# Optimization experiments

Hardware: AMD Instinct MI355X
Metric: run time of the kernel (lower is better)

The kernel has to match this reference:

```python
import jax, jax.numpy as jnp
import numpy as np

T, B, N, C = 4, 16, 256, 512
H = 8
HID = 4 * C
TAU = 2.0
EPS = 1e-5
SCALE = 0.125

@jax.custom_vjp
def spike_fn(x):
    return (x >= 0.0).astype(x.dtype)

def _spike_fwd(x):
    return spike_fn(x), x

def _spike_bwd(x, g):
    alpha = 4.0  # spikingjelly sigmoid surrogate default
    s = jax.nn.sigmoid(alpha * x)
    return (g * alpha * s * (1.0 - s),)

spike_fn.defvjp(_spike_fwd, _spike_bwd)

def lif(x_seq, v_th=1.0):
    # Multi-step LIF: v += (x - v)/tau (decay_input, v_reset=0), hard reset, detach_reset
    def step(v, xt):
        v = v + (xt - v) / TAU
        s = spike_fn(v - v_th)
        v = v * (1.0 - jax.lax.stop_gradient(s))
        return v, s
    _, out = jax.lax.scan(step, jnp.zeros_like(x_seq[0]), x_seq)
    return out

def lin_bn(x2d, w, b, g, beta):
    # Linear then BatchNorm1d (training mode, per-channel stats over all rows).
    # BN on (TB, Cout, N) over (batch, N) == BN on flattened (TB*N, Cout) over axis 0.
    y = x2d @ w.T + b
    mu = jnp.mean(y, axis=0)
    var = jnp.var(y, axis=0)
    return g * (y - mu) * jax.lax.rsqrt(var + EPS) + beta

def setup_inputs() -> dict:
    key = jax.random.key(0)
    ks = jax.random.split(key, 10)
    d = {
        "x": jax.random.normal(ks[0], (T, B, N, C), jnp.float32),
        "s_x": jax.random.normal(ks[1], (T, B, N, C), jnp.float32),
    }
    def lin(k, cout, cin):
        return jax.random.normal(k, (cout, cin), jnp.float32) * 0.02
    d["qw"] = lin(ks[2], C, C); d["qb"] = jnp.zeros((C,), jnp.float32)
    d["qg"] = jnp.ones((C,), jnp.float32); d["qbeta"] = jnp.zeros((C,), jnp.float32)
    d["kw"] = lin(ks[3], C, C); d["kb"] = jnp.zeros((C,), jnp.float32)
    d["kg"] = jnp.ones((C,), jnp.float32); d["kbeta"] = jnp.zeros((C,), jnp.float32)
    d["vw"] = lin(ks[4], C, C); d["vb"] = jnp.zeros((C,), jnp.float32)
    d["vg"] = jnp.ones((C,), jnp.float32); d["vbeta"] = jnp.zeros((C,), jnp.float32)
    d["pw"] = lin(ks[5], C, C); d["pb"] = jnp.zeros((C,), jnp.float32)
    d["pg"] = jnp.ones((C,), jnp.float32); d["pbeta"] = jnp.zeros((C,), jnp.float32)
    d["f1w"] = lin(ks[6], HID, C); d["f1b"] = jnp.zeros((HID,), jnp.float32)
    d["f1g"] = jnp.ones((HID,), jnp.float32); d["f1beta"] = jnp.zeros((HID,), jnp.float32)
    d["f2w"] = lin(ks[7], C, HID); d["f2b"] = jnp.zeros((C,), jnp.float32)
    d["f2g"] = jnp.ones((C,), jnp.float32); d["f2beta"] = jnp.zeros((C,), jnp.float32)
    return d

def _block(x, s_x, qw, qb, qg, qbeta, kw, kb, kg, kbeta, vw, vb, vg, vbeta,
           pw, pb, pg, pbeta, f1w, f1b, f1g, f1beta, f2w, f2b, f2g, f2beta):
    Dh = C // H
    xf = x.reshape(T * B * N, C)
    # SSA (s_x is unused in the source forward)
    q = lif(lin_bn(xf, qw, qb, qg, qbeta).reshape(T, B, N, C))
    k = lif(lin_bn(xf, kw, kb, kg, kbeta).reshape(T, B, N, C))
    v = lin_bn(xf, vw, vb, vg, vbeta).reshape(T, B, N, C)  # v has no LIF in source
    q = q.reshape(T, B, N, H, Dh).transpose(0, 1, 3, 2, 4)  # tbhnd
    k = k.reshape(T, B, N, H, Dh).transpose(0, 1, 3, 2, 4)
    v = v.reshape(T, B, N, H, Dh).transpose(0, 1, 3, 2, 4)
    attn = jnp.einsum('tbhnd,tbhmd->tbhnm', q, k) * SCALE  # no softmax
    o = jnp.einsum('tbhnm,tbhmd->tbhnd', attn, v)
    o = o.transpose(0, 1, 3, 2, 4).reshape(T * B * N, C)
    o = lin_bn(o, pw, pb, pg, pbeta).reshape(T, B, N, C)
    x = x + o
    # MLP
    xf2 = x.reshape(T * B * N, C)
    h = lif(lin_bn(xf2, f1w, f1b, f1g, f1beta).reshape(T, B, N, HID))
    m = lif(lin_bn(h.reshape(T * B * N, HID), f2w, f2b, f2g, f2beta).reshape(T, B, N, C))
    return x + m

def reference(x, s_x, qw, qb, qg, qbeta, kw, kb, kg, kbeta, vw, vb, vg, vbeta,
              pw, pb, pg, pbeta, f1w, f1b, f1g, f1beta, f2w, f2b, f2g, f2beta):
    return _block(x, s_x, qw, qb, qg, qbeta, kw, kb, kg, kbeta, vw, vb, vg, vbeta,
                  pw, pb, pg, pbeta, f1w, f1b, f1g, f1beta, f2w, f2b, f2g, f2beta)
```

## Files before the change

kernel.cpp:

```cpp
#include <hip/hip_runtime.h>
#include <cstdint>

#define T_ 4
#define B_ 16
#define N_ 256
#define C_ 512
#define H_ 8
#define HID_ 2048
#define M_ (T_*B_*N_)
#define BNP_ (B_*N_)

__global__ __launch_bounds__(256, 2)
void gemm_f32_t128(const float* __restrict__ A, const float* __restrict__ W,
                   const float* __restrict__ bias, float* __restrict__ Y,
                   int Nc, int K) {
  __shared__ float As[2][16][132];
  __shared__ float Ws[2][16][132];
  const int tid  = threadIdx.x;
  const int row0 = blockIdx.y * 128;
  const int col0 = blockIdx.x * 128;
  const int tx = tid & 15, ty = tid >> 4;
  const int ar = tid >> 2;
  const int ac = (tid & 3) << 2;

  float acc[8][8];
  #pragma unroll
  for (int i = 0; i < 8; ++i)
    #pragma unroll
    for (int j = 0; j < 8; ++j) acc[i][j] = 0.f;

  const float* Ap0 = A + (size_t)(row0 + ar) * K + ac;
  const float* Ap1 = A + (size_t)(row0 + ar + 64) * K + ac;
  const float* Wp0 = W + (size_t)(col0 + ar) * K + ac;
  const float* Wp1 = W + (size_t)(col0 + ar + 64) * K + ac;

  float4 pa0 = *(const float4*)Ap0;
  float4 pa1 = *(const float4*)Ap1;
  float4 pw0 = *(const float4*)Wp0;
  float4 pw1 = *(const float4*)Wp1;
  As[0][ac+0][ar] = pa0.x; As[0][ac+1][ar] = pa0.y; As[0][ac+2][ar] = pa0.z; As[0][ac+3][ar] = pa0.w;
  As[0][ac+0][ar+64] = pa1.x; As[0][ac+1][ar+64] = pa1.y; As[0][ac+2][ar+64] = pa1.z; As[0][ac+3][ar+64] = pa1.w;
  Ws[0][ac+0][ar] = pw0.x; Ws[0][ac+1][ar] = pw0.y; Ws[0][ac+2][ar] = pw0.z; Ws[0][ac+3][ar] = pw0.w;
  Ws[0][ac+0][ar+64] = pw1.x; Ws[0][ac+1][ar+64] = pw1.y; Ws[0][ac+2][ar+64] = pw1.z; Ws[0][ac+3][ar+64] = pw1.w;
  __syncthreads();

  int buf = 0;
  for (int k0 = 0; k0 < K; k0 += 16) {
    const bool last = (k0 + 16 >= K);
    if (!last) {
      pa0 = *(const float4*)(Ap0 + k0 + 16);
      pa1 = *(const float4*)(Ap1 + k0 + 16);
      pw0 = *(const float4*)(Wp0 + k0 + 16);
      pw1 = *(const float4*)(Wp1 + k0 + 16);
    }
    #pragma unroll
    for (int kk = 0; kk < 16; ++kk) {
      float a[8], b[8];
      *(float4*)&a[0] = *(const float4*)&As[buf][kk][ty*4];
      *(float4*)&a[4] = *(const float4*)&As[buf][kk][64 + ty*4];
      *(float4*)&b[0] = *(const float4*)&Ws[buf][kk][tx*4];
      *(float4*)&b[4] = *(const float4*)&Ws[buf][kk][64 + tx*4];
      #pragma unroll
      for (int i = 0; i < 8; ++i)
        #pragma unroll
        for (int j = 0; j < 8; ++j)
          acc[i][j] = fmaf(a[i], b[j], acc[i][j]);
    }
    if (!last) {
      int nb = buf ^ 1;
      As[nb][ac+0][ar] = pa0.x; As[nb][ac+1][ar] = pa0.y; As[nb][ac+2][ar] = pa0.z; As[nb][ac+3][ar] = pa0.w;
      As[nb][ac+0][ar+64] = pa1.x; As[nb][ac+1][ar+64] = pa1.y; As[nb][ac+2][ar+64] = pa1.z; As[nb][ac+3][ar+64] = pa1.w;
      Ws[nb][ac+0][ar] = pw0.x; Ws[nb][ac+1][ar] = pw0.y; Ws[nb][ac+2][ar] = pw0.z; Ws[nb][ac+3][ar] = pw0.w;
      Ws[nb][ac+0][ar+64] = pw1.x; Ws[nb][ac+1][ar+64] = pw1.y; Ws[nb][ac+2][ar+64] = pw1.z; Ws[nb][ac+3][ar+64] = pw1.w;
      __syncthreads();
      buf = nb;
    }
  }

  #pragma unroll
  for (int ih = 0; ih < 2; ++ih)
    #pragma unroll
    for (int i = 0; i < 4; ++i) {
      size_t r = (size_t)(row0 + ih*64 + ty*4 + i);
      #pragma unroll
      for (int jh = 0; jh < 2; ++jh) {
        int c = col0 + jh*64 + tx*4;
        float4 o4;
        o4.x = acc[ih*4+i][jh*4+0] + bias[c+0];
        o4.y = acc[ih*4+i][jh*4+1] + bias[c+1];
        o4.z = acc[ih*4+i][jh*4+2] + bias[c+2];
        o4.w = acc[ih*4+i][jh*4+3] + bias[c+3];
        *(float4*)(Y + r * Nc + c) = o4;
      }
    }
}

__global__ __launch_bounds__(256, 2)
void gemm_f32_qk(const float* __restrict__ A,
                 const float* __restrict__ Wq, const float* __restrict__ bq,
                 const float* __restrict__ Wk, const float* __restrict__ bk,
                 float* __restrict__ Yq, float* __restrict__ Yk,
                 int Nc, int K) {
  __shared__ float As[2][16][68];
  __shared__ float Wqs[2][16][132];
  __shared__ float Wks[2][16][132];
  const int tid  = threadIdx.x;
  const int row0 = blockIdx.y * 64;
  const int col0 = blockIdx.x * 128;
  const int tx = tid & 15, ty = tid >> 4;
  const int ar = tid >> 2;
  const int ac = (tid & 3) << 2;

  float accq[4][8], acck[4][8];
  #pragma unroll
  for (int i = 0; i < 4; ++i)
    #pragma unroll
    for (int j = 0; j < 8; ++j) { accq[i][j] = 0.f; acck[i][j] = 0.f; }

  const float* Ap   = A  + (size_t)(row0 + ar) * K + ac;
  const float* Wqp0 = Wq + (size_t)(col0 + ar) * K + ac;
  const float* Wqp1 = Wq + (size_t)(col0 + ar + 64) * K + ac;
  const float* Wkp0 = Wk + (size_t)(col0 + ar) * K + ac;
  const float* Wkp1 = Wk + (size_t)(col0 + ar + 64) * K + ac;

  float4 pa  = *(const float4*)Ap;
  float4 pq0 = *(const float4*)Wqp0;
  float4 pq1 = *(const float4*)Wqp1;
  float4 pk0 = *(const float4*)Wkp0;
  float4 pk1 = *(const float4*)Wkp1;
  As[0][ac+0][ar] = pa.x; As[0][ac+1][ar] = pa.y; As[0][ac+2][ar] = pa.z; As[0][ac+3][ar] = pa.w;
  Wqs[0][ac+0][ar] = pq0.x; Wqs[0][ac+1][ar] = pq0.y; Wqs[0][ac+2][ar] = pq0.z; Wqs[0][ac+3][ar] = pq0.w;
  Wqs[0][ac+0][ar+64] = pq1.x; Wqs[0][ac+1][ar+64] = pq1.y; Wqs[0][ac+2][ar+64] = pq1.z; Wqs[0][ac+3][ar+64] = pq1.w;
  Wks[0][ac+0][ar] = pk0.x; Wks[0][ac+1][ar] = pk0.y; Wks[0][ac+2][ar] = pk0.z; Wks[0][ac+3][ar] = pk0.w;
  Wks[0][ac+0][ar+64] = pk1.x; Wks[0][ac+1][ar+64] = pk1.y; Wks[0][ac+2][ar+64] = pk1.z; Wks[0][ac+3][ar+64] = pk1.w;
  __syncthreads();

  int buf = 0;
  for (int k0 = 0; k0 < K; k0 += 16) {
    const bool last = (k0 + 16 >= K);
    if (!last) {
      pa  = *(const float4*)(Ap   + k0 + 16);
      pq0 = *(const float4*)(Wqp0 + k0 + 16);
      pq1 = *(const float4*)(Wqp1 + k0 + 16);
      pk0 = *(const float4*)(Wkp0 + k0 + 16);
      pk1 = *(const float4*)(Wkp1 + k0 + 16);
    }
    #pragma unroll
    for (int kk = 0; kk < 16; ++kk) {
      float4 av = *(const float4*)&As[buf][kk][ty*4];
      float a[4] = {av.x, av.y, av.z, av.w};
      float b[8];
      *(float4*)&b[0] = *(const float4*)&Wqs[buf][kk][tx*4];
      *(float4*)&b[4] = *(const float4*)&Wqs[buf][kk][64 + tx*4];
      #pragma unroll
      for (int i = 0; i < 4; ++i)
        #pragma unroll
        for (int j = 0; j < 8; ++j)
          accq[i][j] = fmaf(a[i], b[j], accq[i][j]);
      *(float4*)&b[0] = *(const float4*)&Wks[buf][kk][tx*4];
      *(float4*)&b[4] = *(const float4*)&Wks[buf][kk][64 + tx*4];
      #pragma unroll
      for (int i = 0; i < 4; ++i)
        #pragma unroll
        for (int j = 0; j < 8; ++j)
          acck[i][j] = fmaf(a[i], b[j], acck[i][j]);
    }
    if (!last) {
      int nb = buf ^ 1;
      As[nb][ac+0][ar] = pa.x; As[nb][ac+1][ar] = pa.y; As[nb][ac+2][ar] = pa.z; As[nb][ac+3][ar] = pa.w;
      Wqs[nb][ac+0][ar] = pq0.x; Wqs[nb][ac+1][ar] = pq0.y; Wqs[nb][ac+2][ar] = pq0.z; Wqs[nb][ac+3][ar] = pq0.w;
      Wqs[nb][ac+0][ar+64] = pq1.x; Wqs[nb][ac+1][ar+64] = pq1.y; Wqs[nb][ac+2][ar+64] = pq1.z; Wqs[nb][ac+3][ar+64] = pq1.w;
      Wks[nb][ac+0][ar] = pk0.x; Wks[nb][ac+1][ar] = pk0.y; Wks[nb][ac+2][ar] = pk0.z; Wks[nb][ac+3][ar] = pk0.w;
      Wks[nb][ac+0][ar+64] = pk1.x; Wks[nb][ac+1][ar+64] = pk1.y; Wks[nb][ac+2][ar+64] = pk1.z; Wks[nb][ac+3][ar+64] = pk1.w;
      __syncthreads();
      buf = nb;
    }
  }

  #pragma unroll
  for (int i = 0; i < 4; ++i) {
    size_t r = (size_t)(row0 + ty*4 + i);
    #pragma unroll
    for (int jh = 0; jh < 2; ++jh) {
      int c = col0 + jh*64 + tx*4;
      float4 oq, ok;
      oq.x = accq[i][jh*4+0] + bq[c+0];
      oq.y = accq[i][jh*4+1] + bq[c+1];
      oq.z = accq[i][jh*4+2] + bq[c+2];
      oq.w = accq[i][jh*4+3] + bq[c+3];
      *(float4*)(Yq + r * Nc + c) = oq;
      ok.x = acck[i][jh*4+0] + bk[c+0];
      ok.y = acck[i][jh*4+1] + bk[c+1];
      ok.z = acck[i][jh*4+2] + bk[c+2];
      ok.w = acck[i][jh*4+3] + bk[c+3];
      *(float4*)(Yk + r * Nc + c) = ok;
    }
  }
}

__global__ __launch_bounds__(256, 2)
void gemm_f64_v3(const float* __restrict__ A, const float* __restrict__ W,
                 const float* __restrict__ bias, float* __restrict__ Y,
                 int Nc, int K) {
  __shared__ double As[2][16][68];
  __shared__ double Ws[2][16][132];
  const int tid  = threadIdx.x;
  const int row0 = blockIdx.y * 64;
  const int col0 = blockIdx.x * 128;
  const int tx = tid & 15, ty = tid >> 4;
  const int lr = tid >> 2;
  const int lk = (tid & 3) << 2;

  double acc[4][8];
  #pragma unroll
  for (int i = 0; i < 4; ++i)
    #pragma unroll
    for (int j = 0; j < 8; ++j) acc[i][j] = 0.0;

  const float* Ap  = A + (size_t)(row0 + lr) * K + lk;
  const float* Wp0 = W + (size_t)(col0 + lr) * K + lk;
  const float* Wp1 = W + (size_t)(col0 + lr + 64) * K + lk;

  float4 pa  = *(const float4*)Ap;
  float4 pw0 = *(const float4*)Wp0;
  float4 pw1 = *(const float4*)Wp1;
  As[0][lk+0][lr] = (double)pa.x; As[0][lk+1][lr] = (double)pa.y;
  As[0][lk+2][lr] = (double)pa.z; As[0][lk+3][lr] = (double)pa.w;
  Ws[0][lk+0][lr] = (double)pw0.x; Ws[0][lk+1][lr] = (double)pw0.y;
  Ws[0][lk+2][lr] = (double)pw0.z; Ws[0][lk+3][lr] = (double)pw0.w;
  Ws[0][lk+0][lr+64] = (double)pw1.x; Ws[0][lk+1][lr+64] = (double)pw1.y;
  Ws[0][lk+2][lr+64] = (double)pw1.z; Ws[0][lk+3][lr+64] = (double)pw1.w;
  __syncthreads();

  int buf = 0;
  for (int k0 = 0; k0 < K; k0 += 16) {
    const bool last = (k0 + 16 >= K);
    if (!last) {
      pa  = *(const float4*)(Ap  + k0 + 16);
      pw0 = *(const float4*)(Wp0 + k0 + 16);
      pw1 = *(const float4*)(Wp1 + k0 + 16);
    }
    #pragma unroll
    for (int kk = 0; kk < 16; ++kk) {
      double a[4], b[8];
      *(double2*)&a[0] = *(const double2*)&As[buf][kk][ty*4];
      *(double2*)&a[2] = *(const double2*)&As[buf][kk][ty*4+2];
      *(double2*)&b[0] = *(const double2*)&Ws[buf][kk][tx*2];
      *(double2*)&b[2] = *(const double2*)&Ws[buf][kk][32 + tx*2];
      *(double2*)&b[4] = *(const double2*)&Ws[buf][kk][64 + tx*2];
      *(double2*)&b[6] = *(const double2*)&Ws[buf][kk][96 + tx*2];
      #pragma unroll
      for (int i = 0; i < 4; ++i)
        #pragma unroll
        for (int j = 0; j < 8; ++j)
          acc[i][j] = fma(a[i], b[j], acc[i][j]);
    }
    if (!last) {
      int nb = buf ^ 1;
      As[nb][lk+0][lr] = (double)pa.x; As[nb][lk+1][lr] = (double)pa.y;
      As[nb][lk+2][lr] = (double)pa.z; As[nb][lk+3][lr] = (double)pa.w;
      Ws[nb][lk+0][lr] = (double)pw0.x; Ws[nb][lk+1][lr] = (double)pw0.y;
      Ws[nb][lk+2][lr] = (double)pw0.z; Ws[nb][lk+3][lr] = (double)pw0.w;
      Ws[nb][lk+0][lr+64] = (double)pw1.x; Ws[nb][lk+1][lr+64] = (double)pw1.y;
      Ws[nb][lk+2][lr+64] = (double)pw1.z; Ws[nb][lk+3][lr+64] = (double)pw1.w;
      __syncthreads();
      buf = nb;
    }
  }

  #pragma unroll
  for (int i = 0; i < 4; ++i) {
    size_t r = (size_t)(row0 + ty*4 + i);
    #pragma unroll
    for (int g = 0; g < 4; ++g) {
      int c = col0 + g*32 + tx*2;
      float2 o2;
      o2.x = (float)(acc[i][g*2+0] + (double)bias[c+0]);
      o2.y = (float)(acc[i][g*2+1] + (double)bias[c+1]);
      *(float2*)(Y + r * Nc + c) = o2;
    }
  }
}

__global__ __launch_bounds__(256)
void col_stats_partial(const float* __restrict__ Y, int Nc,
                       float* __restrict__ psum, float* __restrict__ psq) {
  const int r0 = blockIdx.x * 32;
  for (int c = threadIdx.x; c < Nc; c += 256) {
    float s = 0.f, q = 0.f;
    const float* p = Y + (size_t)r0 * Nc + c;
    for (int r = 0; r < 32; ++r) {
      float v = p[(size_t)r * Nc];
      s += v;
      q = fmaf(v, v, q);
    }
    psum[(size_t)blockIdx.x * Nc + c] = s;
    psq [(size_t)blockIdx.x * Nc + c] = q;
  }
}

__global__ void col_stats_final(const float* __restrict__ psum, const float* __restrict__ psq,
                                int Nc, const float* __restrict__ g, const float* __restrict__ beta,
                                float* __restrict__ chp) {
  int c = blockIdx.x * blockDim.x + threadIdx.x;
  if (c >= Nc) return;
  double s = 0.0, q = 0.0;
  for (int p = 0; p < 512; ++p) {
    s += (double)psum[(size_t)p * Nc + c];
    q += (double)psq [(size_t)p * Nc + c];
  }
  double mean = s / (double)M_;
  double var  = q / (double)M_ - mean * mean;
  float alpha = g[c] / sqrtf((float)var + 1e-5f);
  chp[2*c]   = alpha;
  chp[2*c+1] = fmaf(-(float)mean, alpha, beta[c]);
}

__global__ void col_stats_final_f64(const float* __restrict__ psum, const float* __restrict__ psq,
                                    int Nc, const float* __restrict__ g, const float* __restrict__ beta,
                                    double* __restrict__ chpd) {
  int c = blockIdx.x * blockDim.x + threadIdx.x;
  if (c >= Nc) return;
  double s = 0.0, q = 0.0;
  for (int p = 0; p < 512; ++p) {
    s += (double)psum[(size_t)p * Nc + c];
    q += (double)psq [(size_t)p * Nc + c];
  }
  double mean = s / (double)M_;
  double var  = q / (double)M_ - mean * mean;
  double alpha = (double)g[c] / sqrt(var + 1e-5);
  chpd[2*c]   = alpha;
  chpd[2*c+1] = (double)beta[c] - mean * alpha;
}

__global__ __launch_bounds__(256)
void bnlif_mask(const float* __restrict__ Y, const float* __restrict__ chp,
                unsigned long long* __restrict__ mask) {
  int lane = threadIdx.x & 63;
  int u  = blockIdx.x * 4 + (threadIdx.x >> 6);
  int bn = u >> 3, cg = u & 7;
  int c  = cg * 64 + lane;
  float alpha = chp[2*c], bb = chp[2*c+1];
  float v = 0.f;
  #pragma unroll
  for (int t = 0; t < 4; ++t) {
    float y  = Y[((size_t)(t * BNP_ + bn)) * C_ + c];
    float uu = fmaf(y, alpha, bb);
    v = v + (uu - v) * 0.5f;
    bool sp = (v >= 1.0f);
    unsigned long long m = __ballot(sp);
    if (sp) v = 0.f;
    if (lane == 0) mask[((size_t)(t * BNP_ + bn)) * H_ + cg] = m;
  }
}

__global__ void bn_apply_f64(const float* __restrict__ Y, const double* __restrict__ chpd,
                             float* __restrict__ out) {
  const long total4 = (long)M_ * C_ / 4;
  for (long i = (long)blockIdx.x * blockDim.x + threadIdx.x; i < total4;
       i += (long)gridDim.x * blockDim.x) {
    int c4 = (int)(i & (C_/4 - 1)) * 4;
    float4 y = ((const float4*)Y)[i];
    float4 r;
    r.x = (float)fma((double)y.x, chpd[2*(c4+0)], chpd[2*(c4+0)+1]);
    r.y = (float)fma((double)y.y, chpd[2*(c4+1)], chpd[2*(c4+1)+1]);
    r.z = (float)fma((double)y.z, chpd[2*(c4+2)], chpd[2*(c4+2)+1]);
    r.w = (float)fma((double)y.w, chpd[2*(c4+3)], chpd[2*(c4+3)+1]);
    ((float4*)out)[i] = r;
  }
}

__global__ void bn_residual_f64(const float* __restrict__ Y, const double* __restrict__ chpd,
                                const float* __restrict__ x, float* __restrict__ out) {
  const long total4 = (long)M_ * C_ / 4;
  for (long i = (long)blockIdx.x * blockDim.x + threadIdx.x; i < total4;
       i += (long)gridDim.x * blockDim.x) {
    int c4 = (int)(i & (C_/4 - 1)) * 4;
    float4 y = ((const float4*)Y)[i];
    float4 xv = ((const float4*)x)[i];
    float4 r;
    r.x = (float)((double)xv.x + fma((double)y.x, chpd[2*(c4+0)], chpd[2*(c4+0)+1]));
    r.y = (float)((double)xv.y + fma((double)y.y, chpd[2*(c4+1)], chpd[2*(c4+1)+1]));
    r.z = (float)((double)xv.z + fma((double)y.z, chpd[2*(c4+2)], chpd[2*(c4+2)+1]));
    r.w = (float)((double)xv.w + fma((double)y.w, chpd[2*(c4+3)], chpd[2*(c4+3)+1]));
    ((float4*)out)[i] = r;
  }
}

__global__ __launch_bounds__(256)
void bnlif_inplace(float* __restrict__ Y, const float* __restrict__ chp) {
  int c  = blockIdx.x * 256 + threadIdx.x;
  int bn = blockIdx.y;
  float alpha = chp[2*c], bb = chp[2*c+1];
  float v = 0.f;
  #pragma unroll
  for (int t = 0; t < 4; ++t) {
    size_t idx = ((size_t)(t * BNP_ + bn)) * HID_ + c;
    float uu = fmaf(Y[idx], alpha, bb);
    v = v + (uu - v) * 0.5f;
    bool sp = (v >= 1.f);
    Y[idx] = sp ? 1.f : 0.f;
    if (sp) v = 0.f;
  }
}

__global__ __launch_bounds__(256)
void bnlif_final(const float* __restrict__ Y, const float* __restrict__ chp,
                 const float* __restrict__ xo, float* __restrict__ out) {
  int c  = blockIdx.x * 256 + threadIdx.x;
  int bn = blockIdx.y;
  float alpha = chp[2*c], bb = chp[2*c+1];
  float v = 0.f;
  #pragma unroll
  for (int t = 0; t < 4; ++t) {
    size_t idx = ((size_t)(t * BNP_ + bn)) * C_ + c;
    float uu = fmaf(Y[idx], alpha, bb);
    v = v + (uu - v) * 0.5f;
    bool sp = (v >= 1.f);
    out[idx] = xo[idx] + (sp ? 1.f : 0.f);
    if (sp) v = 0.f;
  }
}

__global__ __launch_bounds__(256)
void attn_kernel_f64(const unsigned long long* __restrict__ qmask,
                     const unsigned long long* __restrict__ kmask,
                     const float* __restrict__ v, float* __restrict__ o) {
  __shared__ unsigned long long km[256];
  __shared__ float vt[256][64];
  int rb  = blockIdx.x & 3;
  int tbh = blockIdx.x >> 2;
  int h   = tbh & 7, tb = tbh >> 3;
  int tid = threadIdx.x;

  km[tid] = kmask[(size_t)(tb * 256 + tid) * H_ + h];
  const float* vbase = v + (size_t)tb * 256 * C_ + h * 64;
  #pragma unroll
  for (int i = 0; i < 16; ++i) {
    int f = i * 256 + tid;
    int r = f >> 4, c4 = f & 15;
    *(float4*)&vt[r][c4 * 4] = *(const float4*)(vbase + (size_t)r * C_ + c4 * 4);
  }
  int lane = tid & 63, w = tid >> 6;
  int nr = lane & 15, dg = lane >> 4;
  int n  = rb * 64 + w * 16 + nr;
  unsigned long long qm = qmask[(size_t)(tb * 256 + n) * H_ + h];
  __syncthreads();

  double acc[16];
  #pragma unroll
  for (int j = 0; j < 16; ++j) acc[j] = 0.0;

  for (int m = 0; m < 256; ++m) {
    double s = (double)__popcll(qm & km[m]) * 0.125;
    #pragma unroll
    for (int j = 0; j < 4; ++j) {
      float4 vv = *(const float4*)&vt[m][dg * 16 + j * 4];
      acc[j*4+0] = fma(s, (double)vv.x, acc[j*4+0]);
      acc[j*4+1] = fma(s, (double)vv.y, acc[j*4+1]);
      acc[j*4+2] = fma(s, (double)vv.z, acc[j*4+2]);
      acc[j*4+3] = fma(s, (double)vv.w, acc[j*4+3]);
    }
  }
  float* orow = o + (size_t)(tb * 256 + n) * C_ + h * 64 + dg * 16;
  #pragma unroll
  for (int j = 0; j < 4; ++j)
    *(float4*)(orow + j * 4) = make_float4((float)acc[j*4], (float)acc[j*4+1],
                                           (float)acc[j*4+2], (float)acc[j*4+3]);
}

extern "C" void kernel_launch(void* const* d_in, const int* in_sizes, int n_in,
                              void* d_out, int out_size, void* d_ws, size_t ws_size,
                              hipStream_t stream) {
  const float* x    = (const float*)d_in[0];
  const float* qw   = (const float*)d_in[2];
  const float* qb   = (const float*)d_in[3];
  const float* qg   = (const float*)d_in[4];
  const float* qbe  = (const float*)d_in[5];
  const float* kw   = (const float*)d_in[6];
  const float* kb   = (const float*)d_in[7];
  const float* kg   = (const float*)d_in[8];
  const float* kbe  = (const float*)d_in[9];
  const float* vw   = (const float*)d_in[10];
  const float* vb   = (const float*)d_in[11];
  const float* vg   = (const float*)d_in[12];
  const float* vbe  = (const float*)d_in[13];
  const float* pw   = (const float*)d_in[14];
  const float* pb   = (const float*)d_in[15];
  const float* pg   = (const float*)d_in[16];
  const float* pbe  = (const float*)d_in[17];
  const float* f1w  = (const float*)d_in[18];
  const float* f1b  = (const float*)d_in[19];
  const float* f1g  = (const float*)d_in[20];
  const float* f1be = (const float*)d_in[21];
  const float* f2w  = (const float*)d_in[22];
  const float* f2b  = (const float*)d_in[23];
  const float* f2g  = (const float*)d_in[24];
  const float* f2be = (const float*)d_in[25];

  char* ws = (char*)d_ws;
  float* bufY = (float*)(ws);
  float* bufK = bufY + 8388608;
  float* bufV = (float*)(ws + 134217728ull);
  float* bufO = (float*)(ws + 167772160ull);
  unsigned long long* qmask = (unsigned long long*)(ws + 201326592ull);
  unsigned long long* kmask = (unsigned long long*)(ws + 202375168ull);
  float* psum = (float*)(ws + 203423744ull);
  float* psq  = (float*)(ws + 207618048ull);
  float* chp  = (float*)(ws + 211812352ull);
  double* chpd = (double*)(ws + 211828736ull);

  float* out = (float*)d_out;

  gemm_f32_qk<<<dim3(4,256), 256, 0, stream>>>(x, qw, qb, kw, kb, bufY, bufK, C_, C_);
  col_stats_partial<<<512, 256, 0, stream>>>(bufY, C_, psum, psq);
  col_stats_final<<<2, 256, 0, stream>>>(psum, psq, C_, qg, qbe, chp);
  bnlif_mask<<<8192, 256, 0, stream>>>(bufY, chp, qmask);
  col_stats_partial<<<512, 256, 0, stream>>>(bufK, C_, psum, psq);
  col_stats_final<<<2, 256, 0, stream>>>(psum, psq, C_, kg, kbe, chp);
  bnlif_mask<<<8192, 256, 0, stream>>>(bufK, chp, kmask);
  gemm_f64_v3<<<dim3(4,256), 256, 0, stream>>>(x, vw, vb, bufY, C_, C_);
  col_stats_partial<<<512, 256, 0, stream>>>(bufY, C_, psum, psq);
  col_stats_final_f64<<<2, 256, 0, stream>>>(psum, psq, C_, vg, vbe, chpd);
  bn_apply_f64<<<2048, 256, 0, stream>>>(bufY, chpd, bufV);
  attn_kernel_f64<<<2048, 256, 0, stream>>>(qmask, kmask, bufV, bufO);
  gemm_f64_v3<<<dim3(4,256), 256, 0, stream>>>(bufO, pw, pb, bufY, C_, C_);
  col_stats_partial<<<512, 256, 0, stream>>>(bufY, C_, psum, psq);
  col_stats_final_f64<<<2, 256, 0, stream>>>(psum, psq, C_, pg, pbe, chpd);
  bn_residual_f64<<<2048, 256, 0, stream>>>(bufY, chpd, x, bufO);
  gemm_f32_t128<<<dim3(16,128), 256, 0, stream>>>(bufO, f1w, f1b, bufY, HID_, C_);
  col_stats_partial<<<512, 256, 0, stream>>>(bufY, HID_, psum, psq);
  col_stats_final<<<8, 256, 0, stream>>>(psum, psq, HID_, f1g, f1be, chp);
  bnlif_inplace<<<dim3(8,4096), 256, 0, stream>>>(bufY, chp);
  gemm_f32_t128<<<dim3(4,128), 256, 0, stream>>>(bufY, f2w, f2b, bufV, C_, HID_);
  col_stats_partial<<<512, 256, 0, stream>>>(bufV, C_, psum, psq);
  col_stats_final<<<2, 256, 0, stream>>>(psum, psq, C_, f2g, f2be, chp);
  bnlif_final<<<dim3(2,4096), 256, 0, stream>>>(bufV, chp, bufO, out);
}
```

Measured before the change: 1.937 ms.

## Pack MLP hidden spikes into bitmasks and run sparse f2 GEMM; widen f1 tile

The hidden LIF now writes a 64-bit ballot bitmask per row and 64 channels instead of a dense 0/1 float matrix. The second MLP linear becomes a sparse gather-accumulate that adds only the weight rows whose spike bit is set, so it skips multiplies by zero and reads far less activation memory. The f1 GEMM tile is also widened to 128x256 with a 8x16 accumulator per thread to improve reuse. The tradeoffs are divergent, data-dependent loops in the sparse kernel, a different summation order from the dense GEMM, and higher register pressure in the wider f1 tile.

Result: slower. 2.433 ms (+25.6%).

```diff
diff --git a/kernel.cpp b/kernel.cpp
--- a/kernel.cpp
+++ b/kernel.cpp
@@ -11,37 +11,43 @@
 #define BNP_ (B_*N_)
 
 __global__ __launch_bounds__(256, 2)
-void gemm_f32_t128(const float* __restrict__ A, const float* __restrict__ W,
+void gemm_f32_t256(const float* __restrict__ A, const float* __restrict__ W,
                    const float* __restrict__ bias, float* __restrict__ Y,
                    int Nc, int K) {
   __shared__ float As[2][16][132];
-  __shared__ float Ws[2][16][132];
+  __shared__ float Ws[2][16][260];
   const int tid  = threadIdx.x;
   const int row0 = blockIdx.y * 128;
-  const int col0 = blockIdx.x * 128;
+  const int col0 = blockIdx.x * 256;
   const int tx = tid & 15, ty = tid >> 4;
   const int ar = tid >> 2;
   const int ac = (tid & 3) << 2;
 
-  float acc[8][8];
+  float acc[8][16];
   #pragma unroll
   for (int i = 0; i < 8; ++i)
     #pragma unroll
-    for (int j = 0; j < 8; ++j) acc[i][j] = 0.f;
+    for (int j = 0; j < 16; ++j) acc[i][j] = 0.f;
 
   const float* Ap0 = A + (size_t)(row0 + ar) * K + ac;
   const float* Ap1 = A + (size_t)(row0 + ar + 64) * K + ac;
   const float* Wp0 = W + (size_t)(col0 + ar) * K + ac;
   const float* Wp1 = W + (size_t)(col0 + ar + 64) * K + ac;
+  const float* Wp2 = W + (size_t)(col0 + ar + 128) * K + ac;
+  const float* Wp3 = W + (size_t)(col0 + ar + 192) * K + ac;
 
   float4 pa0 = *(const float4*)Ap0;
   float4 pa1 = *(const float4*)Ap1;
   float4 pw0 = *(const float4*)Wp0;
   float4 pw1 = *(const float4*)Wp1;
+  float4 pw2 = *(const float4*)Wp2;
+  float4 pw3 = *(const float4*)Wp3;
   As[0][ac+0][ar] = pa0.x; As[0][ac+1][ar] = pa0.y; As[0][ac+2][ar] = pa0.z; As[0][ac+3][ar] = pa0.w;
   As[0][ac+0][ar+64] = pa1.x; As[0][ac+1][ar+64] = pa1.y; As[0][ac+2][ar+64] = pa1.z; As[0][ac+3][ar+64] = pa1.w;
   Ws[0][ac+0][ar] = pw0.x; Ws[0][ac+1][ar] = pw0.y; Ws[0][ac+2][ar] = pw0.z; Ws[0][ac+3][ar] = pw0.w;
   Ws[0][ac+0][ar+64] = pw1.x; Ws[0][ac+1][ar+64] = pw1.y; Ws[0][ac+2][ar+64] = pw1.z; Ws[0][ac+3][ar+64] = pw1.w;
+  Ws[0][ac+0][ar+128] = pw2.x; Ws[0][ac+1][ar+128] = pw2.y; Ws[0][ac+2][ar+128] = pw2.z; Ws[0][ac+3][ar+128] = pw2.w;
+  Ws[0][ac+0][ar+192] = pw3.x; Ws[0][ac+1][ar+192] = pw3.y; Ws[0][ac+2][ar+192] = pw3.z; Ws[0][ac+3][ar+192] = pw3.w;
   __syncthreads();
 
   int buf = 0;
@@ -52,18 +58,22 @@
       pa1 = *(const float4*)(Ap1 + k0 + 16);
       pw0 = *(const float4*)(Wp0 + k0 + 16);
       pw1 = *(const float4*)(Wp1 + k0 + 16);
+      pw2 = *(const float4*)(Wp2 + k0 + 16);
+      pw3 = *(const float4*)(Wp3 + k0 + 16);
     }
     #pragma unroll
     for (int kk = 0; kk < 16; ++kk) {
-      float a[8], b[8];
+      float a[8], b[16];
       *(float4*)&a[0] = *(const float4*)&As[buf][kk][ty*4];
       *(float4*)&a[4] = *(const float4*)&As[buf][kk][64 + ty*4];
-      *(float4*)&b[0] = *(const float4*)&Ws[buf][kk][tx*4];
-      *(float4*)&b[4] = *(const float4*)&Ws[buf][kk][64 + tx*4];
+      *(float4*)&b[0]  = *(const float4*)&Ws[buf][kk][tx*4];
+      *(float4*)&b[4]  = *(const float4*)&Ws[buf][kk][64 + tx*4];
+      *(float4*)&b[8]  = *(const float4*)&Ws[buf][kk][128 + tx*4];
+      *(float4*)&b[12] = *(const float4*)&Ws[buf][kk][192 + tx*4];
       #pragma unroll
       for (int i = 0; i < 8; ++i)
         #pragma unroll
-        for (int j = 0; j < 8; ++j)
+        for (int j = 0; j < 16; ++j)
           acc[i][j] = fmaf(a[i], b[j], acc[i][j]);
     }
     if (!last) {
@@ -72,6 +82,8 @@
       As[nb][ac+0][ar+64] = pa1.x; As[nb][ac+1][ar+64] = pa1.y; As[nb][ac+2][ar+64] = pa1.z; As[nb][ac+3][ar+64] = pa1.w;
       Ws[nb][ac+0][ar] = pw0.x; Ws[nb][ac+1][ar] = pw0.y; Ws[nb][ac+2][ar] = pw0.z; Ws[nb][ac+3][ar] = pw0.w;
       Ws[nb][ac+0][ar+64] = pw1.x; Ws[nb][ac+1][ar+64] = pw1.y; Ws[nb][ac+2][ar+64] = pw1.z; Ws[nb][ac+3][ar+64] = pw1.w;
+      Ws[nb][ac+0][ar+128] = pw2.x; Ws[nb][ac+1][ar+128] = pw2.y; Ws[nb][ac+2][ar+128] = pw2.z; Ws[nb][ac+3][ar+128] = pw2.w;
+      Ws[nb][ac+0][ar+192] = pw3.x; Ws[nb][ac+1][ar+192] = pw3.y; Ws[nb][ac+2][ar+192] = pw3.z; Ws[nb][ac+3][ar+192] = pw3.w;
       __syncthreads();
       buf = nb;
     }
@@ -83,7 +95,7 @@
     for (int i = 0; i < 4; ++i) {
       size_t r = (size_t)(row0 + ih*64 + ty*4 + i);
       #pragma unroll
-      for (int jh = 0; jh < 2; ++jh) {
+      for (int jh = 0; jh < 4; ++jh) {
         int c = col0 + jh*64 + tx*4;
         float4 o4;
         o4.x = acc[ih*4+i][jh*4+0] + bias[c+0];
@@ -93,6 +105,79 @@
         *(float4*)(Y + r * Nc + c) = o4;
       }
     }
+}
+
+__global__ __launch_bounds__(256, 2)
+void gemm_f32_f2sparse(const unsigned long long* __restrict__ hmask,
+                       const float* __restrict__ W, const float* __restrict__ bias,
+                       float* __restrict__ Y) {
+  __shared__ float Ws[2][64][132];
+  __shared__ unsigned long long Ms[2][64];
+  const int tid  = threadIdx.x;
+  const int row0 = blockIdx.y * 64;
+  const int col0 = blockIdx.x * 128;
+  const int lane = tid & 63, wv = tid >> 6;
+  const int sc  = tid >> 1;
+  const int skq = (tid & 1) * 32;
+
+  float acc[16][2];
+  #pragma unroll
+  for (int i = 0; i < 16; ++i) { acc[i][0] = 0.f; acc[i][1] = 0.f; }
+
+  const float* Wp = W + (size_t)(col0 + sc) * 2048 + skq;
+
+  #pragma unroll
+  for (int i = 0; i < 8; ++i) {
+    float4 w4 = *(const float4*)(Wp + 4*i);
+    Ws[0][skq+4*i+0][sc] = w4.x; Ws[0][skq+4*i+1][sc] = w4.y;
+    Ws[0][skq+4*i+2][sc] = w4.z; Ws[0][skq+4*i+3][sc] = w4.w;
+  }
+  if (tid < 64) Ms[0][tid] = hmask[(size_t)(row0 + tid) * 32];
+  __syncthreads();
+
+  int buf = 0;
+  for (int ch = 0; ch < 32; ++ch) {
+    const bool last = (ch == 31);
+    float4 pw[8];
+    unsigned long long pm = 0;
+    if (!last) {
+      #pragma unroll
+      for (int i = 0; i < 8; ++i) pw[i] = *(const float4*)(Wp + (ch+1)*64 + 4*i);
+      if (tid < 64) pm = hmask[(size_t)(row0 + tid) * 32 + ch + 1];
+    }
+    #pragma unroll
+    for (int ri = 0; ri < 16; ++ri) {
+      unsigned long long m = Ms[buf][wv*16 + ri];
+      while (m) {
+        int k = __builtin_ctzll(m);
+        m &= m - 1;
+        float2 b2 = *(const float2*)&Ws[buf][k][lane*2];
+        acc[ri][0] = acc[ri][0] + b2.x;
+        acc[ri][1] = acc[ri][1] + b2.y;
+      }
+    }
+    if (!last) {
+      int nb = buf ^ 1;
+      #pragma unroll
+      for (int i = 0; i < 8; ++i) {
+        Ws[nb][skq+4*i+0][sc] = pw[i].x; Ws[nb][skq+4*i+1][sc] = pw[i].y;
+        Ws[nb][skq+4*i+2][sc] = pw[i].z; Ws[nb][skq+4*i+3][sc] = pw[i].w;
+      }
+      if (tid < 64) Ms[nb][tid] = pm;
+      __syncthreads();
+      buf = nb;
+    }
+  }
+
+  #pragma unroll
+  for (int ri = 0; ri < 16; ++ri) {
+    size_t r = (size_t)(row0 + wv*16 + ri);
+    int c = col0 + lane*2;
+    float2 o2;
+    o2.x = acc[ri][0] + bias[c+0];
+    o2.y = acc[ri][1] + bias[c+1];
+    *(float2*)(Y + r * 512 + c) = o2;
+  }
 }
 
 __global__ __launch_bounds__(256, 2)
@@ -388,19 +473,23 @@
 }
 
 __global__ __launch_bounds__(256)
-void bnlif_inplace(float* __restrict__ Y, const float* __restrict__ chp) {
+void bnlif_hmask(const float* __restrict__ Y, const float* __restrict__ chp,
+                 unsigned long long* __restrict__ hmask) {
   int c  = blockIdx.x * 256 + threadIdx.x;
   int bn = blockIdx.y;
+  int lane = threadIdx.x & 63;
+  int word = blockIdx.x * 4 + (threadIdx.x >> 6);
   float alpha = chp[2*c], bb = chp[2*c+1];
   float v = 0.f;
   #pragma unroll
   for (int t = 0; t < 4; ++t) {
-    size_t idx = ((size_t)(t * BNP_ + bn)) * HID_ + c;
-    float uu = fmaf(Y[idx], alpha, bb);
+    size_t row = (size_t)(t * BNP_ + bn);
+    float uu = fmaf(Y[row * HID_ + c], alpha, bb);
     v = v + (uu - v) * 0.5f;
     bool sp = (v >= 1.f);
-    Y[idx] = sp ? 1.f : 0.f;
+    unsigned long long m = __ballot(sp);
     if (sp) v = 0.f;
+    if (lane == 0) hmask[row * 32 + word] = m;
   }
 }
 
@@ -509,6 +598,7 @@
   float* psq  = (float*)(ws + 207618048ull);
   float* chp  = (float*)(ws + 211812352ull);
   double* chpd = (double*)(ws + 211828736ull);
+  unsigned long long* hmask = (unsigned long long*)bufV;
 
   float* out = (float*)d_out;
 
@@ -528,12 +618,12 @@
   col_stats_partial<<<512, 256, 0, stream>>>(bufY, C_, psum, psq);
   col_stats_final_f64<<<2, 256, 0, stream>>>(psum, psq, C_, pg, pbe, chpd);
   bn_residual_f64<<<2048, 256, 0, stream>>>(bufY, chpd, x, bufO);
-  gemm_f32_t128<<<dim3(16,128), 256, 0, stream>>>(bufO, f1w, f1b, bufY, HID_, C_);
+  gemm_f32_t256<<<dim3(8,128), 256, 0, stream>>>(bufO, f1w, f1b, bufY, HID_, C_);
   col_stats_partial<<<512, 256, 0, stream>>>(bufY, HID_, psum, psq);
   col_stats_final<<<8, 256, 0, stream>>>(psum, psq, HID_, f1g, f1be, chp);
-  bnlif_inplace<<<dim3(8,4096), 256, 0, stream>>>(bufY, chp);
-  gemm_f32_t128<<<dim3(4,128), 256, 0, stream>>>(bufY, f2w, f2b, bufV, C_, HID_);
-  col_stats_partial<<<512, 256, 0, stream>>>(bufV, C_, psum, psq);
+  bnlif_hmask<<<dim3(8,4096), 256, 0, stream>>>(bufY, chp, hmask);
+  gemm_f32_f2sparse<<<dim3(4,256), 256, 0, stream>>>(hmask, f2w, f2b, bufY);
+  col_stats_partial<<<512, 256, 0, stream>>>(bufY, C_, psum, psq);
   col_stats_final<<<2, 256, 0, stream>>>(psum, psq, C_, f2g, f2be, chp);
-  bnlif_final<<<dim3(2,4096), 256, 0, stream>>>(bufV, chp, bufO, out);
-}
+  bnlif_final<<<dim3(2,4096), 256, 0, stream>>>(bufY, chp, bufO, out);
+}
```
